# Performance work log

Hardware: AMD Instinct MI355X
Metric: run time of the kernel (lower is better)

The kernel has to match this reference:

```python
import jax, jax.numpy as jnp
import numpy as np

L, D, N = 4096, 1024, 16  # seq_len, d_model, hiddens_per_input


def setup_inputs() -> dict:
    key = jax.random.key(0)
    ks = jax.random.split(key, 9)
    x = jax.random.normal(ks[0], (L, D), dtype=jnp.float32)
    # Delta param (pre-softplus); softplus(Delta) > 0 is the discretization step
    Delta = jax.random.normal(ks[1], (D,), dtype=jnp.float32)
    # A stored as (re, im); default scheme uses A_re = -1 (stable), theta in [0, 2pi)
    A_re = -(0.5 + 0.5 * jax.random.uniform(ks[2], (D, N), dtype=jnp.float32))
    A_im = jax.random.uniform(ks[3], (D, N), dtype=jnp.float32) * 2.0 * jnp.pi
    scale = 1.0 / jnp.sqrt(jnp.float32(D))  # matrix_init: randn / sqrt(shape[0])
    B_re = jax.random.normal(ks[4], (D, N), dtype=jnp.float32) * scale
    B_im = jax.random.normal(ks[5], (D, N), dtype=jnp.float32) * scale
    C_re = jax.random.normal(ks[6], (D, N), dtype=jnp.float32) * scale
    C_im = jax.random.normal(ks[7], (D, N), dtype=jnp.float32) * scale
    D_param = jax.random.normal(ks[8], (D,), dtype=jnp.float32) * scale
    return {"x": x, "Delta": Delta, "A_re": A_re, "A_im": A_im,
            "B_re": B_re, "B_im": B_im, "C_re": C_re, "C_im": C_im,
            "D_param": D_param}


def _binary_operator_diag(q_i, q_j):
    """Associative op for diagonal linear recurrence h_j = A_j h_{j-1} + b_j."""
    A_i, b_i = q_i
    A_j, b_j = q_j
    return (A_j * A_i, A_j * b_i + b_j)


def reference(x, Delta, A_re, A_im, B_re, B_im, C_re, C_im, D_param):
    Bc = B_re + 1j * B_im                      # (D, N) complex
    Cc = C_re + 1j * C_im                      # (D, N) complex
    Ac = A_re + 1j * A_im                      # (D, N) complex
    dt = jax.nn.softplus(Delta)                # (D,)
    # shared_Delta=True branch: Lambda = exp(dt[:, None] * A), repeated over L
    Lam = jnp.exp(dt[:, None] * Ac)            # (D, N) complex
    Lambda_elements = jnp.broadcast_to(Lam[None, :, :], (x.shape[0], *Lam.shape))
    # Bu = einsum('D, D N, L D -> L D N', dt, B, x)
    Bu_elements = jnp.einsum('D,DN,LD->LDN', dt.astype(Bc.dtype), Bc,
                             x.astype(Bc.dtype))
    _, hidden_states = jax.lax.associative_scan(
        _binary_operator_diag, (Lambda_elements, Bu_elements))  # (L, D, N)
    out = jnp.einsum('LDN,DN->LD', hidden_states, Cc) + D_param[None, :] * x
    return out.real
```

## Files before the change

kernel.cpp:

```cpp
#include <hip/hip_runtime.h>
#include <math.h>

constexpr int L   = 4096;
constexpr int D   = 1024;
constexpr int N   = 16;
constexpr int CPB = 2;
constexpr int NB  = D / CPB;
constexpr int NCB = 128;
constexpr int T   = L / NCB;
constexpr int NT  = 512;

typedef float v2 __attribute__((ext_vector_type(2)));

__device__ __forceinline__ float softplus_f(float v) {
    return fmaxf(v, 0.0f) + log1pf(expf(-fabsf(v)));
}

__device__ __forceinline__ void lam_fast(float ar, float ai, float dt,
                                         float& lr, float& li) {
    float e = __expf(ar * dt);
    float s, c;
    __sincosf(ai * dt, &s, &c);
    lr = e * c;
    li = e * s;
}

__device__ __forceinline__ v2 vfma(v2 a, v2 b, v2 c) {
    return __builtin_elementwise_fma(a, b, c);
}

__global__ __launch_bounds__(NT, 4) void k_fused(
    const float* __restrict__ x,
    const float* __restrict__ Delta,
    const float* __restrict__ A_re, const float* __restrict__ A_im,
    const float* __restrict__ B_re, const float* __restrict__ B_im,
    const float* __restrict__ C_re, const float* __restrict__ C_im,
    const float* __restrict__ Dp,
    float* __restrict__ out)
{
    __shared__ float  xs[T * 256];
    __shared__ float2 sums[NCB * 32];

    const int b  = blockIdx.x;
    const int d0 = (b & 7) * 128 + (b >> 3) * 2;
    const int t  = threadIdx.x;

    {
        const int sct = t & 127;
        const int si  = t >> 7;
        float2 v[8];
        #pragma unroll
        for (int k = 0; k < 8; ++k) {
            int l = sct * T + si * 8 + k;
            v[k] = *(const float2*)(x + (size_t)l * D + d0);
        }
        #pragma unroll
        for (int k = 0; k < 8; ++k) {
            int il = si * 8 + k;
            *(float2*)&xs[il * 256 + sct * 2] = v[k];
        }
    }

    const int h  = t & 1;
    const int dd = (t >> 1) & 1;
    const int ct = t >> 2;
    const int d  = d0 + dd;
    const float dt = softplus_f(Delta[d]);

    v2 LR[4], LI[4];
    {
        const int base = d * N + h * 8;
        float4 a0 = *(const float4*)(A_re + base);
        float4 a1 = *(const float4*)(A_re + base + 4);
        float4 m0 = *(const float4*)(A_im + base);
        float4 m1 = *(const float4*)(A_im + base + 4);
        const float ar[8] = {a0.x, a0.y, a0.z, a0.w, a1.x, a1.y, a1.z, a1.w};
        const float ai[8] = {m0.x, m0.y, m0.z, m0.w, m1.x, m1.y, m1.z, m1.w};
        #pragma unroll
        for (int p = 0; p < 4; ++p) {
            float lr0, li0, lr1, li1;
            lam_fast(ar[2 * p], ai[2 * p], dt, lr0, li0);
            lam_fast(ar[2 * p + 1], ai[2 * p + 1], dt, lr1, li1);
            LR[p] = (v2){lr0, lr1};
            LI[p] = (v2){li0, li1};
        }
    }
    __syncthreads();

    v2 GR[4] = {(v2)0, (v2)0, (v2)0, (v2)0};
    v2 GI[4] = {(v2)0, (v2)0, (v2)0, (v2)0};
    #pragma unroll 4
    for (int i = 0; i < T; ++i) {
        float xv = xs[i * 256 + ct * 2 + dd];
        v2 XV = (v2){xv, xv};
        #pragma unroll
        for (int p = 0; p < 4; ++p) {
            v2 t2 = vfma(-LI[p], GI[p], XV);
            v2 nr = vfma(LR[p], GR[p], t2);
            GI[p] = vfma(LR[p], GI[p], LI[p] * GR[p]);
            GR[p] = nr;
        }
    }
    {
        float2* sp = &sums[ct * 32 + dd * 16 + h * 8];
        #pragma unroll
        for (int p = 0; p < 4; ++p) {
            sp[2 * p]     = make_float2(GR[p].x, GI[p].x);
            sp[2 * p + 1] = make_float2(GR[p].y, GI[p].y);
        }
    }
    __syncthreads();

    if (t < 32) {
        const int dd2 = t >> 4, n2 = t & 15;
        const int d2  = d0 + dd2;
        const float dt2 = softplus_f(Delta[d2]);
        float lr, li;
        lam_fast(A_re[d2 * N + n2], A_im[d2 * N + n2], dt2, lr, li);
        #pragma unroll
        for (int k = 0; k < 5; ++k) {
            float nr = lr * lr - li * li;
            li = 2.0f * lr * li;
            lr = nr;
        }
        float cr = 0.0f, ci = 0.0f;
        #pragma unroll
        for (int c0 = 0; c0 < NCB; c0 += 16) {
            float2 sv[16];
            #pragma unroll
            for (int u = 0; u < 16; ++u) sv[u] = sums[(c0 + u) * 32 + t];
            #pragma unroll
            for (int u = 0; u < 16; ++u) {
                sums[(c0 + u) * 32 + t] = make_float2(cr, ci);
                float nr = fmaf(lr, cr, fmaf(-li, ci, sv[u].x));
                ci = fmaf(lr, ci, fmaf(li, cr, sv[u].y));
                cr = nr;
            }
        }
    }

    v2 CR[4], CI[4];
    {
        const int base = d * N + h * 8;
        float4 b0 = *(const float4*)(B_re + base);
        float4 b1 = *(const float4*)(B_re + base + 4);
        float4 e0 = *(const float4*)(B_im + base);
        float4 e1 = *(const float4*)(B_im + base + 4);
        float4 f0 = *(const float4*)(C_re + base);
        float4 f1 = *(const float4*)(C_re + base + 4);
        float4 g0 = *(const float4*)(C_im + base);
        float4 g1 = *(const float4*)(C_im + base + 4);
        const float br[8] = {b0.x, b0.y, b0.z, b0.w, b1.x, b1.y, b1.z, b1.w};
        const float bi[8] = {e0.x, e0.y, e0.z, e0.w, e1.x, e1.y, e1.z, e1.w};
        const float cr[8] = {f0.x, f0.y, f0.z, f0.w, f1.x, f1.y, f1.z, f1.w};
        const float ci[8] = {g0.x, g0.y, g0.z, g0.w, g1.x, g1.y, g1.z, g1.w};
        #pragma unroll
        for (int p = 0; p < 4; ++p) {
            CR[p] = (v2){dt * (cr[2*p] * br[2*p] - ci[2*p] * bi[2*p]),
                         dt * (cr[2*p+1] * br[2*p+1] - ci[2*p+1] * bi[2*p+1])};
            CI[p] = (v2){dt * (cr[2*p] * bi[2*p] + ci[2*p] * br[2*p]),
                         dt * (cr[2*p+1] * bi[2*p+1] + ci[2*p+1] * br[2*p+1])};
        }
    }
    const float dpv = Dp[d];
    __syncthreads();

    {
        const float2* cp = &sums[ct * 32 + dd * 16 + h * 8];
        #pragma unroll
        for (int p = 0; p < 4; ++p) {
            float2 c0 = cp[2 * p], c1 = cp[2 * p + 1];
            GR[p] = (v2){c0.x, c1.x};
            GI[p] = (v2){c0.y, c1.y};
        }
    }
    #pragma unroll 4
    for (int ib = 0; ib < T / 2; ++ib) {
        float keep = 0.0f;
        #pragma unroll
        for (int u = 0; u < 2; ++u) {
            int i = ib * 2 + u;
            float xv = xs[i * 256 + ct * 2 + dd];
            v2 XV = (v2){xv, xv};
            v2 ACC = (v2)0;
            #pragma unroll
            for (int p = 0; p < 4; ++p) {
                v2 t2 = vfma(-LI[p], GI[p], XV);
                v2 nr = vfma(LR[p], GR[p], t2);
                GI[p] = vfma(LR[p], GI[p], LI[p] * GR[p]);
                GR[p] = nr;
                ACC = vfma(CR[p], GR[p], ACC);
                ACC = vfma(-CI[p], GI[p], ACC);
            }
            float acc = ACC.x + ACC.y;
            acc += __shfl_xor(acc, 1);
            acc = fmaf(dpv, xv, acc);
            keep = (h == u) ? acc : keep;
        }
        out[(size_t)(ct * T + ib * 2 + h) * D + d] = keep;
    }
}

extern "C" void kernel_launch(void* const* d_in, const int* in_sizes, int n_in,
                              void* d_out, int out_size, void* d_ws, size_t ws_size,
                              hipStream_t stream) {
    const float* x     = (const float*)d_in[0];
    const float* Delta = (const float*)d_in[1];
    const float* A_re  = (const float*)d_in[2];
    const float* A_im  = (const float*)d_in[3];
    const float* B_re  = (const float*)d_in[4];
    const float* B_im  = (const float*)d_in[5];
    const float* C_re  = (const float*)d_in[6];
    const float* C_im  = (const float*)d_in[7];
    const float* Dp    = (const float*)d_in[8];
    float* out = (float*)d_out;

    k_fused<<<NB, NT, 0, stream>>>(x, Delta, A_re, A_im, B_re, B_im,
                                   C_re, C_im, Dp, out);
}
```

Before: 106.0 us.

## Process four channels per block with float4 x loads and shuffle-transposed float4 stores

Doubles channels per block from 2 to 4 and the block size from 512 to 1024 threads, halving the grid. x rows are now read as 16-byte float4s, and outputs are gathered across the four channel lanes with xor shuffles so each thread writes a float4 row segment instead of scattered scalars. The goal is wider, better-coalesced global reads and writes. In exchange it adds shuffles, and the runtime-indexed local array f[dd] may spill to scratch. Register pressure also rises, since launch_bounds(1024,4) is kept unchanged.

```diff
diff --git a/kernel.cpp b/kernel.cpp
--- a/kernel.cpp
+++ b/kernel.cpp
@@ -4,11 +4,11 @@
 constexpr int L   = 4096;
 constexpr int D   = 1024;
 constexpr int N   = 16;
-constexpr int CPB = 2;
+constexpr int CPB = 4;
 constexpr int NB  = D / CPB;
 constexpr int NCB = 128;
 constexpr int T   = L / NCB;
-constexpr int NT  = 512;
+constexpr int NT  = 1024;
 
 typedef float v2 __attribute__((ext_vector_type(2)));
 
@@ -38,32 +38,30 @@
     const float* __restrict__ Dp,
     float* __restrict__ out)
 {
-    __shared__ float  xs[T * 256];
-    __shared__ float2 sums[NCB * 32];
+    __shared__ float  xs[T * 512];
+    __shared__ float2 sums[NCB * 64];
 
     const int b  = blockIdx.x;
-    const int d0 = (b & 7) * 128 + (b >> 3) * 2;
+    const int d0 = (b & 7) * 128 + (b >> 3) * 4;
     const int t  = threadIdx.x;
 
     {
         const int sct = t & 127;
         const int si  = t >> 7;
-        float2 v[8];
-        #pragma unroll
-        for (int k = 0; k < 8; ++k) {
-            int l = sct * T + si * 8 + k;
-            v[k] = *(const float2*)(x + (size_t)l * D + d0);
-        }
-        #pragma unroll
-        for (int k = 0; k < 8; ++k) {
-            int il = si * 8 + k;
-            *(float2*)&xs[il * 256 + sct * 2] = v[k];
-        }
+        float4 v[4];
+        #pragma unroll
+        for (int k = 0; k < 4; ++k) {
+            int l = sct * T + si * 4 + k;
+            v[k] = *(const float4*)(x + (size_t)l * D + d0);
+        }
+        #pragma unroll
+        for (int k = 0; k < 4; ++k)
+            *(float4*)&xs[(si * 4 + k) * 512 + sct * 4] = v[k];
     }
 
     const int h  = t & 1;
-    const int dd = (t >> 1) & 1;
-    const int ct = t >> 2;
+    const int dd = (t >> 1) & 3;
+    const int ct = t >> 3;
     const int d  = d0 + dd;
     const float dt = softplus_f(Delta[d]);
 
@@ -91,7 +89,7 @@
     v2 GI[4] = {(v2)0, (v2)0, (v2)0, (v2)0};
     #pragma unroll 4
     for (int i = 0; i < T; ++i) {
-        float xv = xs[i * 256 + ct * 2 + dd];
+        float xv = xs[i * 512 + ct * 4 + dd];
         v2 XV = (v2){xv, xv};
         #pragma unroll
         for (int p = 0; p < 4; ++p) {
@@ -102,7 +100,7 @@
         }
     }
     {
-        float2* sp = &sums[ct * 32 + dd * 16 + h * 8];
+        float2* sp = &sums[ct * 64 + dd * 16 + h * 8];
         #pragma unroll
         for (int p = 0; p < 4; ++p) {
             sp[2 * p]     = make_float2(GR[p].x, GI[p].x);
@@ -111,7 +109,7 @@
     }
     __syncthreads();
 
-    if (t < 32) {
+    if (t < 64) {
         const int dd2 = t >> 4, n2 = t & 15;
         const int d2  = d0 + dd2;
         const float dt2 = softplus_f(Delta[d2]);
@@ -128,10 +126,10 @@
         for (int c0 = 0; c0 < NCB; c0 += 16) {
             float2 sv[16];
             #pragma unroll
-            for (int u = 0; u < 16; ++u) sv[u] = sums[(c0 + u) * 32 + t];
+            for (int u = 0; u < 16; ++u) sv[u] = sums[(c0 + u) * 64 + t];
             #pragma unroll
             for (int u = 0; u < 16; ++u) {
-                sums[(c0 + u) * 32 + t] = make_float2(cr, ci);
+                sums[(c0 + u) * 64 + t] = make_float2(cr, ci);
                 float nr = fmaf(lr, cr, fmaf(-li, ci, sv[u].x));
                 ci = fmaf(lr, ci, fmaf(li, cr, sv[u].y));
                 cr = nr;
@@ -166,7 +164,7 @@
     __syncthreads();
 
     {
-        const float2* cp = &sums[ct * 32 + dd * 16 + h * 8];
+        const float2* cp = &sums[ct * 64 + dd * 16 + h * 8];
         #pragma unroll
         for (int p = 0; p < 4; ++p) {
             float2 c0 = cp[2 * p], c1 = cp[2 * p + 1];
@@ -174,30 +172,40 @@
             GI[p] = (v2){c0.y, c1.y};
         }
     }
-    #pragma unroll 4
-    for (int ib = 0; ib < T / 2; ++ib) {
-        float keep = 0.0f;
-        #pragma unroll
-        for (int u = 0; u < 2; ++u) {
-            int i = ib * 2 + u;
-            float xv = xs[i * 256 + ct * 2 + dd];
-            v2 XV = (v2){xv, xv};
-            v2 ACC = (v2)0;
+    #pragma unroll
+    for (int ob = 0; ob < T / 8; ++ob) {
+        float Vh[4];
+        #pragma unroll
+        for (int ib = 0; ib < 4; ++ib) {
             #pragma unroll
-            for (int p = 0; p < 4; ++p) {
-                v2 t2 = vfma(-LI[p], GI[p], XV);
-                v2 nr = vfma(LR[p], GR[p], t2);
-                GI[p] = vfma(LR[p], GI[p], LI[p] * GR[p]);
-                GR[p] = nr;
-                ACC = vfma(CR[p], GR[p], ACC);
-                ACC = vfma(-CI[p], GI[p], ACC);
+            for (int u = 0; u < 2; ++u) {
+                int i = ob * 8 + ib * 2 + u;
+                float xv = xs[i * 512 + ct * 4 + dd];
+                v2 XV = (v2){xv, xv};
+                v2 ACC = (v2)0;
+                #pragma unroll
+                for (int p = 0; p < 4; ++p) {
+                    v2 t2 = vfma(-LI[p], GI[p], XV);
+                    v2 nr = vfma(LR[p], GR[p], t2);
+                    GI[p] = vfma(LR[p], GI[p], LI[p] * GR[p]);
+                    GR[p] = nr;
+                    ACC = vfma(CR[p], GR[p], ACC);
+                    ACC = vfma(-CI[p], GI[p], ACC);
+                }
+                float acc = ACC.x + ACC.y;
+                acc += __shfl_xor(acc, 1);
+                acc = fmaf(dpv, xv, acc);
+                if (u == h) Vh[ib] = acc;
             }
-            float acc = ACC.x + ACC.y;
-            acc += __shfl_xor(acc, 1);
-            acc = fmaf(dpv, xv, acc);
-            keep = (h == u) ? acc : keep;
-        }
-        out[(size_t)(ct * T + ib * 2 + h) * D + d] = keep;
+        }
+        float f[4];
+        f[dd]     = Vh[dd];
+        f[dd ^ 1] = __shfl_xor(Vh[dd ^ 1], 2);
+        f[dd ^ 2] = __shfl_xor(Vh[dd ^ 2], 4);
+        f[dd ^ 3] = __shfl_xor(Vh[dd ^ 3], 6);
+        int row = ct * T + ob * 8 + dd * 2 + h;
+        *(float4*)(out + (size_t)row * D + d0) =
+            make_float4(f[0], f[1], f[2], f[3]);
     }
 }
 
```

After: 102.8 us. 1.03x faster.
